# Performance work log

Hardware: AMD Instinct MI355X
Metric: run time of the kernel (lower is better)

## Reference

```python
import jax, jax.numpy as jnp
import numpy as np

N = 100_000      # total nodes
E = 1_600_000    # total edges
G = 32           # number of graphs in batch
IN = 100         # in_channels
H = 64           # hidden_channels
L = 3            # num_layers
EPS = 1e-5       # BatchNorm eps


def setup_inputs() -> dict:
    key = jax.random.key(0)
    ks = jax.random.split(key, 16)
    x = jax.random.normal(ks[0], (N, IN), jnp.float32)
    edge_index = jax.random.randint(ks[1], (2, E), 0, N)
    edge_weight = jax.random.uniform(ks[2], (E,), jnp.float32)
    batch = jnp.sort(jax.random.randint(ks[3], (N,), 0, G))
    inp = {"x": x, "edge_index": edge_index, "edge_weight": edge_weight, "batch": batch}
    dims = [IN] + [H] * L
    for i in range(L):
        din, dout = dims[i], dims[i + 1]
        s = 1.0 / np.sqrt(din)
        inp[f"W{i}"] = jax.random.uniform(ks[4 + i], (din, dout), jnp.float32, -s, s)
        inp[f"b{i}"] = jnp.zeros((dout,), jnp.float32)
        inp[f"g{i}"] = jnp.ones((dout,), jnp.float32)   # BN gamma
        inp[f"bt{i}"] = jnp.zeros((dout,), jnp.float32)  # BN beta
        inp[f"rm{i}"] = jnp.zeros((dout,), jnp.float32)  # BN running mean
        inp[f"rv{i}"] = jnp.ones((dout,), jnp.float32)   # BN running var
    return inp


def reference(x, edge_index, edge_weight, batch,
              W0, b0, g0, bt0, rm0, rv0,
              W1, b1, g1, bt1, rm1, rv1,
              W2, b2, g2, bt2, rm2, rv2):
    n = x.shape[0]
    loop = jnp.arange(n)
    src = jnp.concatenate([edge_index[0], loop])
    dst = jnp.concatenate([edge_index[1], loop])
    w = jnp.concatenate([jnp.abs(edge_weight), jnp.ones((n,), x.dtype)])
    # symmetric GCN normalization (deg computed on target / col)
    deg = jax.ops.segment_sum(w, dst, num_segments=n)
    deg_safe = jnp.where(deg > 0, deg, 1.0)
    dinv = jnp.where(deg > 0, jax.lax.rsqrt(deg_safe), 0.0)
    norm = dinv[src] * w * dinv[dst]  # [E+N]

    def gcn_bn_relu(h, W, b, g, bt, rm, rv):
        h = h @ W                              # [N, dout]
        msg = h[src] * norm[:, None]           # gather + scale
        h = jax.ops.segment_sum(msg, dst, num_segments=n) + b  # scatter-add
        h = (h - rm) * jax.lax.rsqrt(rv + EPS) * g + bt        # BN (eval)
        return jnp.maximum(h, 0.0)             # ReLU (dropout off in eval)

    h = x
    for (W, b, g, bt, rm, rv) in [(W0, b0, g0, bt0, rm0, rv0),
                                  (W1, b1, g1, bt1, rm1, rv1),
                                  (W2, b2, g2, bt2, rm2, rv2)]:
        h = gcn_bn_relu(h, W, b, g, bt, rm, rv)

    # mean+add global pooling
    s = jax.ops.segment_sum(h, batch, num_segments=G)
    cnt = jax.ops.segment_sum(jnp.ones((n,), h.dtype), batch, num_segments=G)
    mean = s / jnp.maximum(cnt, 1.0)[:, None]
    return jnp.concatenate([mean, s], axis=-1)  # [G, 2*H]
```

## Files before the change

kernel.cpp:

```cpp
#include <hip/hip_runtime.h>
#include <hip/hip_bf16.h>

#define NN 100000
#define EE 1600000
#define GG 32
#define INC 100
#define HC 64
#define CAP 64
#define BN_EPS 1e-5f
#define NB_POOL 1563
#define WQ 32767.0f
#define NSLICE 8
#define SLICE_N 12500
#define EBLK 6250

typedef __hip_bfloat16 bf16;

__device__ __forceinline__ float bflo(unsigned u) { return __uint_as_float(u << 16); }
__device__ __forceinline__ float bfhi(unsigned u) { return __uint_as_float(u & 0xffff0000u); }
__device__ __forceinline__ unsigned f2bf(float f) {
    unsigned x = __float_as_uint(f);
    return (x + 0x7fffu + ((x >> 16) & 1u)) >> 16;
}
__device__ __forceinline__ unsigned bfpack(float lo, float hi) {
    return f2bf(lo) | (f2bf(hi) << 16);
}


__global__ __launch_bounds__(256) void k_scatter_ell(const int* __restrict__ ei,
                                                     const float* __restrict__ ew,
                                                     int* __restrict__ cur,
                                                     unsigned* __restrict__ epk) {
    unsigned b = blockIdx.x;
    int slice = b & (NSLICE - 1);
    int e = (int)(b >> 3) * 256 + threadIdx.x;
    if (e >= EE) return;
    int d = __builtin_nontemporal_load(&ei[EE + e]);
    int lo = slice * SLICE_N;
    if (d < lo || d >= lo + SLICE_N) return;
    int s = __builtin_nontemporal_load(&ei[e]);
    float w = __builtin_nontemporal_load(&ew[e]);
    int qw = (int)(fabsf(w) * WQ + 0.5f);
    if (qw > 32767) qw = 32767;
    int slot = atomicAdd(&cur[d], 1);
    if (slot < CAP)
        epk[(size_t)d * CAP + slot] = ((unsigned)s << 15) | (unsigned)qw;
}

__global__ __launch_bounds__(256) void k_dinv_ell(const int* __restrict__ cur,
                                                  const unsigned* __restrict__ epk,
                                                  float* __restrict__ dinv) {
    int wid = (blockIdx.x * 256 + threadIdx.x) >> 6;
    int lane = threadIdx.x & 63;
    if (wid >= NN) return;
    int cnt = min(cur[wid], CAP);
    float v = 0.f;
    if (lane < cnt)
        v = (float)(epk[(size_t)wid * CAP + lane] & 0x7fffu) * (1.0f / WQ);
    for (int o = 32; o > 0; o >>= 1) v += __shfl_down(v, o);
    if (lane == 0) dinv[wid] = rsqrtf(v + 1.0f);
}


__device__ __forceinline__ float ldf(const float* p, size_t i) { return p[i]; }
__device__ __forceinline__ float ldf(const bf16* p, size_t i) { return __bfloat162float(p[i]); }

template <int DIN, typename Tin>
__global__ __launch_bounds__(256) void k_gemm(const Tin* __restrict__ X,
                                              const float* __restrict__ W,
                                              const float* __restrict__ dinv,
                                              bf16* __restrict__ Y) {
    __shared__ float Ws[DIN * 64];
    __shared__ float Xs[32 * DIN];
    int row0 = blockIdx.x * 32;
    for (int idx = threadIdx.x; idx < DIN * 64; idx += 256)
        Ws[idx] = W[idx];
    for (int idx = threadIdx.x; idx < 32 * DIN; idx += 256) {
        int r = idx / DIN, k = idx - r * DIN;
        Xs[idx] = ldf(X, (size_t)(row0 + r) * DIN + k);
    }
    __syncthreads();
    int c = threadIdx.x & 63;
    int r0 = threadIdx.x >> 6;
    float acc[8];
#pragma unroll
    for (int j = 0; j < 8; j++) acc[j] = 0.f;
    for (int k = 0; k < DIN; k++) {
        float wv = Ws[k * 64 + c];
#pragma unroll
        for (int j = 0; j < 8; j++)
            acc[j] += Xs[(r0 + j * 4) * DIN + k] * wv;
    }
#pragma unroll
    for (int j = 0; j < 8; j++) {
        int row = row0 + r0 + j * 4;
        Y[(size_t)row * 64 + c] = __float2bfloat16(acc[j] * dinv[row]);
    }
}


__global__ __launch_bounds__(256) void k_gather_gemm(
    const unsigned* __restrict__ hw32, const int* __restrict__ cur,
    const unsigned* __restrict__ epk, const float* __restrict__ dinv,
    const float* __restrict__ bb, const float* __restrict__ gg,
    const float* __restrict__ btp, const float* __restrict__ rmp,
    const float* __restrict__ rvp, const float* __restrict__ W,
    unsigned* __restrict__ out32) {
    __shared__ float Ws[64 * 64];
    __shared__ float hs[8][64];
    int tid = threadIdx.x;
    for (int idx = tid; idx < 64 * 64; idx += 256)
        Ws[idx] = W[idx];

    int lane = tid & 63;
    int l5 = lane & 31;
    int local = (tid >> 6) * 2 + (lane >> 5);
    int n = blockIdx.x * 8 + local;
    float di = dinv[n];
    unsigned us = hw32[(size_t)n * 32 + l5];
    float a0 = bflo(us), b0 = bfhi(us);
    float a1 = 0.f, b1 = 0.f, a2 = 0.f, b2 = 0.f;
    float a3 = 0.f, b3 = 0.f, a4 = 0.f, b4 = 0.f;
    int cnt = min(cur[n], CAP);
    const unsigned* ce = epk + (size_t)n * CAP;
    const float q = 1.0f / WQ;
    unsigned klo = (l5 < cnt) ? ce[l5] : 0u;
    unsigned khi = 0u;
    if (cnt > 32) khi = (32 + l5 < cnt) ? ce[32 + l5] : 0u;
    int p = 0;
    for (; p + 8 <= cnt; p += 8) {
        unsigned base = (p < 32) ? klo : khi;
        int pb = p & 31;
        unsigned k0 = __shfl(base, pb + 0, 32);
        unsigned k1 = __shfl(base, pb + 1, 32);
        unsigned k2 = __shfl(base, pb + 2, 32);
        unsigned k3 = __shfl(base, pb + 3, 32);
        unsigned k4 = __shfl(base, pb + 4, 32);
        unsigned k5 = __shfl(base, pb + 5, 32);
        unsigned k6 = __shfl(base, pb + 6, 32);
        unsigned k7 = __shfl(base, pb + 7, 32);
        unsigned u0 = hw32[(size_t)(k0 >> 15) * 32 + l5];
        unsigned u1 = hw32[(size_t)(k1 >> 15) * 32 + l5];
        unsigned u2 = hw32[(size_t)(k2 >> 15) * 32 + l5];
        unsigned u3 = hw32[(size_t)(k3 >> 15) * 32 + l5];
        unsigned u4 = hw32[(size_t)(k4 >> 15) * 32 + l5];
        unsigned u5 = hw32[(size_t)(k5 >> 15) * 32 + l5];
        unsigned u6 = hw32[(size_t)(k6 >> 15) * 32 + l5];
        unsigned u7 = hw32[(size_t)(k7 >> 15) * 32 + l5];
        float c0 = (float)(k0 & 0x7fffu) * q, c1 = (float)(k1 & 0x7fffu) * q;
        float c2 = (float)(k2 & 0x7fffu) * q, c3 = (float)(k3 & 0x7fffu) * q;
        float c4 = (float)(k4 & 0x7fffu) * q, c5 = (float)(k5 & 0x7fffu) * q;
        float c6 = (float)(k6 & 0x7fffu) * q, c7 = (float)(k7 & 0x7fffu) * q;
        a0 += bflo(u0) * c0; b0 += bfhi(u0) * c0;
        a1 += bflo(u1) * c1; b1 += bfhi(u1) * c1;
        a2 += bflo(u2) * c2; b2 += bfhi(u2) * c2;
        a3 += bflo(u3) * c3; b3 += bfhi(u3) * c3;
        a4 += bflo(u4) * c4; b4 += bfhi(u4) * c4;
        a0 += bflo(u5) * c5; b0 += bfhi(u5) * c5;
        a1 += bflo(u6) * c6; b1 += bfhi(u6) * c6;
        a2 += bflo(u7) * c7; b2 += bfhi(u7) * c7;
    }
    for (; p + 4 <= cnt; p += 4) {
        unsigned base = (p < 32) ? klo : khi;
        int pb = p & 31;
        unsigned k0 = __shfl(base, pb + 0, 32);
        unsigned k1 = __shfl(base, pb + 1, 32);
        unsigned k2 = __shfl(base, pb + 2, 32);
        unsigned k3 = __shfl(base, pb + 3, 32);
        unsigned u0 = hw32[(size_t)(k0 >> 15) * 32 + l5];
        unsigned u1 = hw32[(size_t)(k1 >> 15) * 32 + l5];
        unsigned u2 = hw32[(size_t)(k2 >> 15) * 32 + l5];
        unsigned u3 = hw32[(size_t)(k3 >> 15) * 32 + l5];
        float c0 = (float)(k0 & 0x7fffu) * q, c1 = (float)(k1 & 0x7fffu) * q;
        float c2 = (float)(k2 & 0x7fffu) * q, c3 = (float)(k3 & 0x7fffu) * q;
        a0 += bflo(u0) * c0; b0 += bfhi(u0) * c0;
        a1 += bflo(u1) * c1; b1 += bfhi(u1) * c1;
        a2 += bflo(u2) * c2; b2 += bfhi(u2) * c2;
        a3 += bflo(u3) * c3; b3 += bfhi(u3) * c3;
    }
    for (; p < cnt; ++p) {
        unsigned base = (p < 32) ? klo : khi;
        unsigned k0 = __shfl(base, p & 31, 32);
        unsigned u0 = hw32[(size_t)(k0 >> 15) * 32 + l5];
        float c0 = (float)(k0 & 0x7fffu) * q;
        a0 += bflo(u0) * c0; b0 += bfhi(u0) * c0;
    }
    int cl = l5 * 2, ch = cl + 1;
    float alo = (((a0 + a1) + (a2 + a3)) + a4) * di + bb[cl];
    float ahi = (((b0 + b1) + (b2 + b3)) + b4) * di + bb[ch];
    float slo = gg[cl] * rsqrtf(rvp[cl] + BN_EPS);
    float shi = gg[ch] * rsqrtf(rvp[ch] + BN_EPS);
    hs[local][cl] = fmaxf((alo - rmp[cl]) * slo + btp[cl], 0.f);
    hs[local][ch] = fmaxf((ahi - rmp[ch]) * shi + btp[ch], 0.f);
    __syncthreads();

    int r = tid >> 5;
    int pr = tid & 31;
    int c2 = pr * 2;
    float accl = 0.f, acch = 0.f;
#pragma unroll 8
    for (int k = 0; k < 64; ++k) {
        float h = hs[r][k];
        accl += h * Ws[k * 64 + c2];
        acch += h * Ws[k * 64 + c2 + 1];
    }
    int rn = blockIdx.x * 8 + r;
    float dib = dinv[rn];
    out32[(size_t)rn * 32 + pr] = bfpack(accl * dib, acch * dib);
}


__global__ __launch_bounds__(256) void k_gather_bn(
    const unsigned* __restrict__ hw32, const int* __restrict__ cur,
    const unsigned* __restrict__ epk, const float* __restrict__ dinv,
    const float* __restrict__ bb, const float* __restrict__ gg,
    const float* __restrict__ btp, const float* __restrict__ rmp,
    const float* __restrict__ rvp, unsigned* __restrict__ ho32) {
    int wave = (blockIdx.x * 256 + threadIdx.x) >> 6;
    int lane = threadIdx.x & 63;
    int n = wave * 2 + (lane >> 5);
    int l5 = lane & 31;
    if (n >= NN) return;
    float di = dinv[n];
    unsigned us = hw32[(size_t)n * 32 + l5];
    float a0 = bflo(us), b0 = bfhi(us);
    float a1 = 0.f, b1 = 0.f, a2 = 0.f, b2 = 0.f;
    float a3 = 0.f, b3 = 0.f, a4 = 0.f, b4 = 0.f;
    int cnt = min(cur[n], CAP);
    const unsigned* ce = epk + (size_t)n * CAP;
    const float q = 1.0f / WQ;
    unsigned klo = (l5 < cnt) ? ce[l5] : 0u;
    unsigned khi = 0u;
    if (cnt > 32) khi = (32 + l5 < cnt) ? ce[32 + l5] : 0u;
    int p = 0;
    for (; p + 8 <= cnt; p += 8) {
        unsigned base = (p < 32) ? klo : khi;
        int pb = p & 31;
        unsigned k0 = __shfl(base, pb + 0, 32);
        unsigned k1 = __shfl(base, pb + 1, 32);
        unsigned k2 = __shfl(base, pb + 2, 32);
        unsigned k3 = __shfl(base, pb + 3, 32);
        unsigned k4 = __shfl(base, pb + 4, 32);
        unsigned k5 = __shfl(base, pb + 5, 32);
        unsigned k6 = __shfl(base, pb + 6, 32);
        unsigned k7 = __shfl(base, pb + 7, 32);
        unsigned u0 = hw32[(size_t)(k0 >> 15) * 32 + l5];
        unsigned u1 = hw32[(size_t)(k1 >> 15) * 32 + l5];
        unsigned u2 = hw32[(size_t)(k2 >> 15) * 32 + l5];
        unsigned u3 = hw32[(size_t)(k3 >> 15) * 32 + l5];
        unsigned u4 = hw32[(size_t)(k4 >> 15) * 32 + l5];
        unsigned u5 = hw32[(size_t)(k5 >> 15) * 32 + l5];
        unsigned u6 = hw32[(size_t)(k6 >> 15) * 32 + l5];
        unsigned u7 = hw32[(size_t)(k7 >> 15) * 32 + l5];
        float c0 = (float)(k0 & 0x7fffu) * q, c1 = (float)(k1 & 0x7fffu) * q;
        float c2 = (float)(k2 & 0x7fffu) * q, c3 = (float)(k3 & 0x7fffu) * q;
        float c4 = (float)(k4 & 0x7fffu) * q, c5 = (float)(k5 & 0x7fffu) * q;
        float c6 = (float)(k6 & 0x7fffu) * q, c7 = (float)(k7 & 0x7fffu) * q;
        a0 += bflo(u0) * c0; b0 += bfhi(u0) * c0;
        a1 += bflo(u1) * c1; b1 += bfhi(u1) * c1;
        a2 += bflo(u2) * c2; b2 += bfhi(u2) * c2;
        a3 += bflo(u3) * c3; b3 += bfhi(u3) * c3;
        a4 += bflo(u4) * c4; b4 += bfhi(u4) * c4;
        a0 += bflo(u5) * c5; b0 += bfhi(u5) * c5;
        a1 += bflo(u6) * c6; b1 += bfhi(u6) * c6;
        a2 += bflo(u7) * c7; b2 += bfhi(u7) * c7;
    }
    for (; p + 4 <= cnt; p += 4) {
        unsigned base = (p < 32) ? klo : khi;
        int pb = p & 31;
        unsigned k0 = __shfl(base, pb + 0, 32);
        unsigned k1 = __shfl(base, pb + 1, 32);
        unsigned k2 = __shfl(base, pb + 2, 32);
        unsigned k3 = __shfl(base, pb + 3, 32);
        unsigned u0 = hw32[(size_t)(k0 >> 15) * 32 + l5];
        unsigned u1 = hw32[(size_t)(k1 >> 15) * 32 + l5];
        unsigned u2 = hw32[(size_t)(k2 >> 15) * 32 + l5];
        unsigned u3 = hw32[(size_t)(k3 >> 15) * 32 + l5];
        float c0 = (float)(k0 & 0x7fffu) * q, c1 = (float)(k1 & 0x7fffu) * q;
        float c2 = (float)(k2 & 0x7fffu) * q, c3 = (float)(k3 & 0x7fffu) * q;
        a0 += bflo(u0) * c0; b0 += bfhi(u0) * c0;
        a1 += bflo(u1) * c1; b1 += bfhi(u1) * c1;
        a2 += bflo(u2) * c2; b2 += bfhi(u2) * c2;
        a3 += bflo(u3) * c3; b3 += bfhi(u3) * c3;
    }
    for (; p < cnt; ++p) {
        unsigned base = (p < 32) ? klo : khi;
        unsigned k0 = __shfl(base, p & 31, 32);
        unsigned u0 = hw32[(size_t)(k0 >> 15) * 32 + l5];
        float c0 = (float)(k0 & 0x7fffu) * q;
        a0 += bflo(u0) * c0; b0 += bfhi(u0) * c0;
    }
    int cl = l5 * 2, ch = cl + 1;
    float alo = (((a0 + a1) + (a2 + a3)) + a4) * di + bb[cl];
    float ahi = (((b0 + b1) + (b2 + b3)) + b4) * di + bb[ch];
    float slo = gg[cl] * rsqrtf(rvp[cl] + BN_EPS);
    float shi = gg[ch] * rsqrtf(rvp[ch] + BN_EPS);
    float olo = fmaxf((alo - rmp[cl]) * slo + btp[cl], 0.f);
    float ohi = fmaxf((ahi - rmp[ch]) * shi + btp[ch], 0.f);
    ho32[(size_t)n * 32 + l5] = bfpack(olo, ohi);
}


__global__ __launch_bounds__(64) void k_pool(const bf16* __restrict__ h,
                                             const int* __restrict__ batch,
                                             float* __restrict__ s, float* __restrict__ cntf) {
    int c = threadIdx.x;
    int n0 = blockIdx.x * 64;
    if (n0 >= NN) return;
    int n1 = n0 + 64; if (n1 > NN) n1 = NN;
    float acc = 0.f, cnt = 0.f;
    int gcur = batch[n0];
    for (int i = n0; i < n1; ++i) {
        int gi = batch[i];
        if (gi != gcur) {
            atomicAdd(&s[gcur * 64 + c], acc);
            if (c == 0) atomicAdd(&cntf[gcur], cnt);
            acc = 0.f; cnt = 0.f; gcur = gi;
        }
        acc += __bfloat162float(h[(size_t)i * 64 + c]);
        cnt += 1.f;
    }
    atomicAdd(&s[gcur * 64 + c], acc);
    if (c == 0) atomicAdd(&cntf[gcur], cnt);
}


__global__ void k_out(const float* __restrict__ s, const float* __restrict__ cntf,
                      float* __restrict__ out) {
    int idx = blockIdx.x * 256 + threadIdx.x;
    if (idx >= GG * 128) return;
    int g = idx >> 7, c = idx & 127;
    float v;
    if (c < 64) v = s[g * 64 + c] / fmaxf(cntf[g], 1.f);
    else        v = s[g * 64 + (c - 64)];
    out[idx] = v;
}


extern "C" void kernel_launch(void* const* d_in, const int* in_sizes, int n_in,
                              void* d_out, int out_size, void* d_ws, size_t ws_size,
                              hipStream_t stream) {
    const float* x   = (const float*)d_in[0];
    const int* ei    = (const int*)d_in[1];
    const float* ew  = (const float*)d_in[2];
    const int* batch = (const int*)d_in[3];
    const float *Wp[3], *bp[3], *gp[3], *btp[3], *rmp[3], *rvp[3];
    for (int l = 0; l < 3; ++l) {
        Wp[l]  = (const float*)d_in[4 + 6 * l + 0];
        bp[l]  = (const float*)d_in[4 + 6 * l + 1];
        gp[l]  = (const float*)d_in[4 + 6 * l + 2];
        btp[l] = (const float*)d_in[4 + 6 * l + 3];
        rmp[l] = (const float*)d_in[4 + 6 * l + 4];
        rvp[l] = (const float*)d_in[4 + 6 * l + 5];
    }

    size_t off = 0;
    auto carve = [&](size_t bytes) {
        void* r = (char*)d_ws + off;
        off += (bytes + 255) & ~(size_t)255;
        return r;
    };
    int*      cur    = (int*)     carve(NN * 4);
    float*    dinv   = (float*)   carve(NN * 4);
    unsigned* epk    = (unsigned*)carve((size_t)NN * CAP * 4);
    bf16*     hw     = (bf16*)    carve((size_t)NN * 64 * 2);
    bf16*     ha     = (bf16*)    carve((size_t)NN * 64 * 2);
    float*    pool_s = (float*)   carve(GG * 64 * 4);
    float*    pool_c = (float*)   carve(GG * 4);

    hipMemsetAsync(cur, 0, NN * 4, stream);
    hipMemsetAsync(pool_s, 0, GG * 64 * 4, stream);
    hipMemsetAsync(pool_c, 0, GG * 4, stream);

    int nwblk  = (NN * 64 + 255) / 256;
    int gatblk = NN / 8;
    int gemm_grid = NN / 32;

    k_scatter_ell<<<EBLK * NSLICE, 256, 0, stream>>>(ei, ew, cur, epk);
    k_dinv_ell<<<nwblk, 256, 0, stream>>>(cur, epk, dinv);

    k_gemm<INC, float><<<gemm_grid, 256, 0, stream>>>(x, Wp[0], dinv, hw);
    k_gather_gemm<<<gatblk, 256, 0, stream>>>((unsigned*)hw, cur, epk, dinv,
                                              bp[0], gp[0], btp[0], rmp[0], rvp[0],
                                              Wp[1], (unsigned*)ha);
    k_gather_gemm<<<gatblk, 256, 0, stream>>>((unsigned*)ha, cur, epk, dinv,
                                              bp[1], gp[1], btp[1], rmp[1], rvp[1],
                                              Wp[2], (unsigned*)hw);
    k_gather_bn<<<gatblk, 256, 0, stream>>>((unsigned*)hw, cur, epk, dinv,
                                            bp[2], gp[2], btp[2], rmp[2], rvp[2], (unsigned*)ha);

    k_pool<<<NB_POOL, 64, 0, stream>>>(ha, batch, pool_s, pool_c);
    k_out<<<(GG * 128 + 255) / 256, 256, 0, stream>>>(pool_s, pool_c, (float*)d_out);
}
```

Baseline: 468.2 us.

## Fuse global pooling into final gather kernel and fold pool memsets into dinv

The last gather+BN+ReLU kernel now reduces its 8 nodes per block in shared memory and atomically adds the per-graph partial sums straight into the pool buffers. This removes the bf16 write and re-read of the final activations and the separate k_pool launch. Zeroing of the pool buffers moves into the first block of k_dinv_ell, which drops two memset calls. The trade-off is many more atomics (one 64-wide set per 8 nodes instead of per 64 nodes) and an extra __syncthreads in the gather kernel.

```diff
diff --git a/kernel.cpp b/kernel.cpp
--- a/kernel.cpp
+++ b/kernel.cpp
@@ -8,7 +8,6 @@
 #define HC 64
 #define CAP 64
 #define BN_EPS 1e-5f
-#define NB_POOL 1563
 #define WQ 32767.0f
 #define NSLICE 8
 #define SLICE_N 12500
@@ -47,9 +46,18 @@
         epk[(size_t)d * CAP + slot] = ((unsigned)s << 15) | (unsigned)qw;
 }
 
+
 __global__ __launch_bounds__(256) void k_dinv_ell(const int* __restrict__ cur,
                                                   const unsigned* __restrict__ epk,
-                                                  float* __restrict__ dinv) {
+                                                  float* __restrict__ dinv,
+                                                  float* __restrict__ pool_s,
+                                                  float* __restrict__ pool_c) {
+    if (blockIdx.x == 0) {
+        for (int i = threadIdx.x; i < GG * 64 + GG; i += 256) {
+            if (i < GG * 64) pool_s[i] = 0.f;
+            else             pool_c[i - GG * 64] = 0.f;
+        }
+    }
     int wid = (blockIdx.x * 256 + threadIdx.x) >> 6;
     int lane = threadIdx.x & 63;
     if (wid >= NN) return;
@@ -210,17 +218,21 @@
 }
 
 
-__global__ __launch_bounds__(256) void k_gather_bn(
+__global__ __launch_bounds__(256) void k_gather_pool(
     const unsigned* __restrict__ hw32, const int* __restrict__ cur,
     const unsigned* __restrict__ epk, const float* __restrict__ dinv,
     const float* __restrict__ bb, const float* __restrict__ gg,
     const float* __restrict__ btp, const float* __restrict__ rmp,
-    const float* __restrict__ rvp, unsigned* __restrict__ ho32) {
-    int wave = (blockIdx.x * 256 + threadIdx.x) >> 6;
-    int lane = threadIdx.x & 63;
-    int n = wave * 2 + (lane >> 5);
+    const float* __restrict__ rvp, const int* __restrict__ batch,
+    float* __restrict__ pool_s, float* __restrict__ pool_c) {
+    __shared__ float hs[8][64];
+    __shared__ int sb[8];
+    int tid = threadIdx.x;
+    int lane = tid & 63;
     int l5 = lane & 31;
-    if (n >= NN) return;
+    int local = (tid >> 6) * 2 + (lane >> 5);
+    int n = blockIdx.x * 8 + local;
+    if (l5 == 0) sb[local] = batch[n];
     float di = dinv[n];
     unsigned us = hw32[(size_t)n * 32 + l5];
     float a0 = bflo(us), b0 = bfhi(us);
@@ -295,33 +307,28 @@
     float ahi = (((b0 + b1) + (b2 + b3)) + b4) * di + bb[ch];
     float slo = gg[cl] * rsqrtf(rvp[cl] + BN_EPS);
     float shi = gg[ch] * rsqrtf(rvp[ch] + BN_EPS);
-    float olo = fmaxf((alo - rmp[cl]) * slo + btp[cl], 0.f);
-    float ohi = fmaxf((ahi - rmp[ch]) * shi + btp[ch], 0.f);
-    ho32[(size_t)n * 32 + l5] = bfpack(olo, ohi);
-}
-
-
-__global__ __launch_bounds__(64) void k_pool(const bf16* __restrict__ h,
-                                             const int* __restrict__ batch,
-                                             float* __restrict__ s, float* __restrict__ cntf) {
-    int c = threadIdx.x;
-    int n0 = blockIdx.x * 64;
-    if (n0 >= NN) return;
-    int n1 = n0 + 64; if (n1 > NN) n1 = NN;
-    float acc = 0.f, cnt = 0.f;
-    int gcur = batch[n0];
-    for (int i = n0; i < n1; ++i) {
-        int gi = batch[i];
-        if (gi != gcur) {
-            atomicAdd(&s[gcur * 64 + c], acc);
-            if (c == 0) atomicAdd(&cntf[gcur], cnt);
-            acc = 0.f; cnt = 0.f; gcur = gi;
+    hs[local][cl] = fmaxf((alo - rmp[cl]) * slo + btp[cl], 0.f);
+    hs[local][ch] = fmaxf((ahi - rmp[ch]) * shi + btp[ch], 0.f);
+    __syncthreads();
+
+    if (tid < 64) {
+        int c = tid;
+        float acc = 0.f, cntf_ = 0.f;
+        int gcur = sb[0];
+#pragma unroll
+        for (int i = 0; i < 8; ++i) {
+            int gi = sb[i];
+            if (gi != gcur) {
+                atomicAdd(&pool_s[gcur * 64 + c], acc);
+                if (c == 0) atomicAdd(&pool_c[gcur], cntf_);
+                acc = 0.f; cntf_ = 0.f; gcur = gi;
+            }
+            acc += hs[i][c];
+            cntf_ += 1.f;
         }
-        acc += __bfloat162float(h[(size_t)i * 64 + c]);
-        cnt += 1.f;
-    }
-    atomicAdd(&s[gcur * 64 + c], acc);
-    if (c == 0) atomicAdd(&cntf[gcur], cnt);
+        atomicAdd(&pool_s[gcur * 64 + c], acc);
+        if (c == 0) atomicAdd(&pool_c[gcur], cntf_);
+    }
 }
 
 
@@ -369,15 +376,13 @@
     float*    pool_c = (float*)   carve(GG * 4);
 
     hipMemsetAsync(cur, 0, NN * 4, stream);
-    hipMemsetAsync(pool_s, 0, GG * 64 * 4, stream);
-    hipMemsetAsync(pool_c, 0, GG * 4, stream);
 
     int nwblk  = (NN * 64 + 255) / 256;
     int gatblk = NN / 8;
     int gemm_grid = NN / 32;
 
     k_scatter_ell<<<EBLK * NSLICE, 256, 0, stream>>>(ei, ew, cur, epk);
-    k_dinv_ell<<<nwblk, 256, 0, stream>>>(cur, epk, dinv);
+    k_dinv_ell<<<nwblk, 256, 0, stream>>>(cur, epk, dinv, pool_s, pool_c);
 
     k_gemm<INC, float><<<gemm_grid, 256, 0, stream>>>(x, Wp[0], dinv, hw);
     k_gather_gemm<<<gatblk, 256, 0, stream>>>((unsigned*)hw, cur, epk, dinv,
@@ -386,9 +391,9 @@
     k_gather_gemm<<<gatblk, 256, 0, stream>>>((unsigned*)ha, cur, epk, dinv,
                                               bp[1], gp[1], btp[1], rmp[1], rvp[1],
                                               Wp[2], (unsigned*)hw);
-    k_gather_bn<<<gatblk, 256, 0, stream>>>((unsigned*)hw, cur, epk, dinv,
-                                            bp[2], gp[2], btp[2], rmp[2], rvp[2], (unsigned*)ha);
-
-    k_pool<<<NB_POOL, 64, 0, stream>>>(ha, batch, pool_s, pool_c);
+    k_gather_pool<<<gatblk, 256, 0, stream>>>((unsigned*)hw, cur, epk, dinv,
+                                              bp[2], gp[2], btp[2], rmp[2], rvp[2],
+                                              batch, pool_s, pool_c);
+
     k_out<<<(GG * 128 + 255) / 256, 256, 0, stream>>>(pool_s, pool_c, (float*)d_out);
 }
```

Result: slower. 550.1 us (+17.5%).
